# Kernel optimization log

Measured on AMD Instinct MI355X. Metric: run time of the kernel, lower is better.

Reference implementation:

```python
import jax, jax.numpy as jnp
import numpy as np

D_K = 128
NEG = -1e19

def setup_inputs() -> dict:
    key = jax.random.key(0)
    k1, k2, k3 = jax.random.split(key, 3)
    B, H, S, D = 4, 16, 2048, D_K
    return {
        "query": jax.random.normal(k1, (B, H, S, D), dtype=jnp.float32),
        "key": jax.random.normal(k2, (B, H, S, D), dtype=jnp.float32),
        "value": jax.random.normal(k3, (B, H, S, D), dtype=jnp.float32),
    }

def reference(query, key, value):
    # scores: [B,H,S,S]
    scores = jnp.einsum('bhqd,bhkd->bhqk', query, key) / np.sqrt(D_K).astype(np.float32)
    S = scores.shape[-1]
    # causal mask: 1 above diagonal -> add -1e19 (masked_mha=True, training=True path)
    mask = 1.0 - jnp.tril(jnp.ones((S, S), dtype=scores.dtype))
    scores = scores + mask[None, None, :, :] * NEG
    probs = jax.nn.softmax(scores, axis=-1)
    return jnp.einsum('bhqk,bhkd->bhqd', probs, value)
```

## Files before the change

kernel.cpp:

```cpp
#include <hip/hip_runtime.h>
#include <hip/hip_bf16.h>

typedef __attribute__((ext_vector_type(8))) short bf16x8;
typedef __attribute__((ext_vector_type(4))) float f32x4;

#define LOG2E  1.4426950408889634f
#define QSCALE 0.08838834764831845f

__device__ __forceinline__ short f2bf(float f) {
  union { float f; unsigned u; } x;
  x.f = f;
  unsigned u = x.u;
  u += 0x7fffu + ((u >> 16) & 1u);
  return (short)(u >> 16);
}

__device__ __forceinline__ unsigned packbf(float a, float b) {
  return (unsigned)(unsigned short)f2bf(a) | ((unsigned)(unsigned short)f2bf(b) << 16);
}

__global__ __launch_bounds__(256, 2) void attn_fwd(
    const float* __restrict__ Qg, const float* __restrict__ Kg,
    const float* __restrict__ Vg, float* __restrict__ Og)
{
  __shared__ short K_lds[2][64 * 128];
  __shared__ short V_T[2][128 * 64];

  const int tid  = threadIdx.x;
  const int lane = tid & 63;
  const int wave = tid >> 6;
  const int g    = lane >> 4;
  const int lo   = lane & 15;
  const int lo7  = lo & 7;

  const int bh = blockIdx.x;
  const int qt = 15 - blockIdx.y;
  const int q0 = qt * 128;

  const size_t base = (size_t)bh * 2048 * 128;
  const float* Qb = Qg + base;
  const float* Kb = Kg + base;
  const float* Vb = Vg + base;
  float*       Ob = Og + base;

  const int vd   = tid & 31;
  const int vprb = tid >> 5;

  bf16x8 qf[2][4];
  #pragma unroll
  for (int mt = 0; mt < 2; ++mt) {
    const int row = q0 + wave * 32 + mt * 16 + lo;
    const float* qr = Qb + (size_t)row * 128 + g * 8;
    #pragma unroll
    for (int kb = 0; kb < 4; ++kb) {
      f32x4 a = *(const f32x4*)(qr + kb * 32);
      f32x4 b = *(const f32x4*)(qr + kb * 32 + 4);
      bf16x8 w;
      #pragma unroll
      for (int jj = 0; jj < 4; ++jj) { w[jj] = f2bf(a[jj] * QSCALE); w[4 + jj] = f2bf(b[jj] * QSCALE); }
      qf[mt][kb] = w;
    }
  }

  float m_st[2] = {-3.0e38f, -3.0e38f};
  float l_st[2] = {0.0f, 0.0f};
  f32x4 o_acc[2][8];
  #pragma unroll
  for (int mt = 0; mt < 2; ++mt)
    #pragma unroll
    for (int nd = 0; nd < 8; ++nd) o_acc[mt][nd] = (f32x4){0.f, 0.f, 0.f, 0.f};

  const bool b1 = (g >> 1) & 1;
  const bool b0 = g & 1;

  const int ntiles = 2 * (qt + 1);

  {
    #pragma unroll
    for (int i = 0; i < 4; ++i) {
      const int idx = i * 256 + tid;
      const int kr = idx >> 4, dc16 = idx & 15;
      const float* src = Kb + (size_t)kr * 128 + dc16 * 8;
      f32x4 a = *(const f32x4*)src;
      f32x4 b = *(const f32x4*)(src + 4);
      bf16x8 w;
      #pragma unroll
      for (int jj = 0; jj < 4; ++jj) { w[jj] = f2bf(a[jj]); w[4 + jj] = f2bf(b[jj]); }
      *(bf16x8*)&K_lds[0][kr * 128 + ((dc16 ^ (kr & 7)) * 8)] = w;
    }
    #pragma unroll
    for (int i = 0; i < 4; ++i) {
      const int pr = vprb + i * 8;
      const float* v0 = Vb + (size_t)(2 * pr) * 128 + vd;
      #pragma unroll
      for (int jj = 0; jj < 4; ++jj) {
        const int row = vd + jj * 32;
        const unsigned pk = packbf(v0[jj * 32], v0[jj * 32 + 128]);
        *(unsigned*)&V_T[0][row * 64 + (((pr >> 2) ^ (row & 7)) * 8) + (pr & 3) * 2] = pk;
      }
    }
  }
  __syncthreads();

  int cur = 0;
  for (int t = 0; t < ntiles; ++t) {
    const int kv0 = t * 64;
    const short* Kc = K_lds[cur];
    const short* Vc = V_T[cur];
    short* Kn = K_lds[cur ^ 1];
    short* Vn = V_T[cur ^ 1];

    f32x4 kpa[4], kpb[4];
    float vp[4][4][2];
    const bool have_next = (t + 1 < ntiles);
    if (have_next) {
      const int nkv0 = kv0 + 64;
      #pragma unroll
      for (int i = 0; i < 4; ++i) {
        const int idx = i * 256 + tid;
        const int kr = idx >> 4, dc16 = idx & 15;
        const float* src = Kb + (size_t)(nkv0 + kr) * 128 + dc16 * 8;
        kpa[i] = *(const f32x4*)src;
        kpb[i] = *(const f32x4*)(src + 4);
      }
      #pragma unroll
      for (int i = 0; i < 4; ++i) {
        const int pr = vprb + i * 8;
        const float* v0 = Vb + (size_t)(nkv0 + 2 * pr) * 128 + vd;
        #pragma unroll
        for (int jj = 0; jj < 4; ++jj) { vp[i][jj][0] = v0[jj * 32]; vp[i][jj][1] = v0[jj * 32 + 128]; }
      }
    }
    __builtin_amdgcn_sched_barrier(0);

    if (kv0 <= q0 + wave * 32 + 31) {
      f32x4 s[2][4];
      #pragma unroll
      for (int mt = 0; mt < 2; ++mt)
        #pragma unroll
        for (int nb = 0; nb < 4; ++nb) s[mt][nb] = (f32x4){0.f, 0.f, 0.f, 0.f};

      __builtin_amdgcn_s_setprio(1);
      #pragma unroll
      for (int nb = 0; nb < 4; ++nb) {
        #pragma unroll
        for (int kb = 0; kb < 4; ++kb) {
          bf16x8 kf = *(const bf16x8*)&Kc[(nb * 16 + lo) * 128 + (((kb * 4 + g) ^ lo7) * 8)];
          s[0][nb] = __builtin_amdgcn_mfma_f32_16x16x32_bf16(kf, qf[0][kb], s[0][nb], 0, 0, 0);
          s[1][nb] = __builtin_amdgcn_mfma_f32_16x16x32_bf16(kf, qf[1][kb], s[1][nb], 0, 0, 0);
        }
      }
      __builtin_amdgcn_s_setprio(0);

      if (kv0 + 63 > q0 + wave * 32) {
        #pragma unroll
        for (int mt = 0; mt < 2; ++mt) {
          const int qrow = q0 + wave * 32 + mt * 16 + lo;
          #pragma unroll
          for (int nb = 0; nb < 4; ++nb) {
            const int kvb = kv0 + nb * 16 + g * 4;
            #pragma unroll
            for (int r = 0; r < 4; ++r)
              if (kvb + r > qrow) s[mt][nb][r] = -1.0e30f;
          }
        }
      }

      bf16x8 pfrag[2][2];
      #pragma unroll
      for (int mt = 0; mt < 2; ++mt) {
        float tm = s[mt][0][0];
        #pragma unroll
        for (int nb = 0; nb < 4; ++nb)
          #pragma unroll
          for (int r = 0; r < 4; ++r) tm = fmaxf(tm, s[mt][nb][r]);
        tm = fmaxf(tm, __shfl_xor(tm, 16));
        tm = fmaxf(tm, __shfl_xor(tm, 32));
        const float mn = fmaxf(m_st[mt], tm);
        const float alpha = __builtin_amdgcn_exp2f((m_st[mt] - mn) * LOG2E);
        m_st[mt] = mn;

        float p[4][4];
        float ps = 0.0f;
        #pragma unroll
        for (int nb = 0; nb < 4; ++nb)
          #pragma unroll
          for (int r = 0; r < 4; ++r) {
            p[nb][r] = __builtin_amdgcn_exp2f((s[mt][nb][r] - mn) * LOG2E);
            ps += p[nb][r];
          }
        ps += __shfl_xor(ps, 16);
        ps += __shfl_xor(ps, 32);
        l_st[mt] = l_st[mt] * alpha + ps;
        #pragma unroll
        for (int nd = 0; nd < 8; ++nd)
          #pragma unroll
          for (int r = 0; r < 4; ++r) o_acc[mt][nd][r] *= alpha;

        unsigned pk[2][2][2];
        #pragma unroll
        for (int n1 = 0; n1 < 2; ++n1)
          #pragma unroll
          for (int n0 = 0; n0 < 2; ++n0)
            #pragma unroll
            for (int w = 0; w < 2; ++w)
              pk[n1][n0][w] = packbf(p[n1 * 2 + n0][2 * w], p[n1 * 2 + n0][2 * w + 1]);

        #pragma unroll
        for (int n1 = 0; n1 < 2; ++n1) {
          unsigned q2[2][2];
          #pragma unroll
          for (int w = 0; w < 2; ++w) {
            unsigned a = pk[n1][0][w], b = pk[n1][1][w];
            unsigned recv = __shfl_xor(b1 ? a : b, 32);
            unsigned r0 = b1 ? recv : a;
            unsigned r1 = b1 ? b : recv;
            unsigned recv2 = __shfl_xor(b0 ? r0 : r1, 16);
            q2[0][w] = b0 ? recv2 : r0;
            q2[1][w] = b0 ? r1 : recv2;
          }
          union { bf16x8 v; unsigned u[4]; } fb;
          fb.u[0] = q2[0][0]; fb.u[1] = q2[0][1]; fb.u[2] = q2[1][0]; fb.u[3] = q2[1][1];
          pfrag[mt][n1] = fb.v;
        }
      }

      __builtin_amdgcn_s_setprio(1);
      #pragma unroll
      for (int kb2 = 0; kb2 < 2; ++kb2) {
        #pragma unroll
        for (int nd = 0; nd < 8; ++nd) {
          bf16x8 vf = *(const bf16x8*)&Vc[(nd * 16 + lo) * 64 + (((kb2 * 4 + g) ^ lo7) * 8)];
          o_acc[0][nd] = __builtin_amdgcn_mfma_f32_16x16x32_bf16(vf, pfrag[0][kb2], o_acc[0][nd], 0, 0, 0);
          o_acc[1][nd] = __builtin_amdgcn_mfma_f32_16x16x32_bf16(vf, pfrag[1][kb2], o_acc[1][nd], 0, 0, 0);
        }
      }
      __builtin_amdgcn_s_setprio(0);
    }

    if (have_next) {
      #pragma unroll
      for (int i = 0; i < 4; ++i) {
        const int idx = i * 256 + tid;
        const int kr = idx >> 4, dc16 = idx & 15;
        bf16x8 w;
        #pragma unroll
        for (int jj = 0; jj < 4; ++jj) { w[jj] = f2bf(kpa[i][jj]); w[4 + jj] = f2bf(kpb[i][jj]); }
        *(bf16x8*)&Kn[kr * 128 + ((dc16 ^ (kr & 7)) * 8)] = w;
      }
      #pragma unroll
      for (int i = 0; i < 4; ++i) {
        const int pr = vprb + i * 8;
        #pragma unroll
        for (int jj = 0; jj < 4; ++jj) {
          const int row = vd + jj * 32;
          const unsigned pk = packbf(vp[i][jj][0], vp[i][jj][1]);
          *(unsigned*)&Vn[row * 64 + (((pr >> 2) ^ (row & 7)) * 8) + (pr & 3) * 2] = pk;
        }
      }
    }
    __syncthreads();
    cur ^= 1;
  }

  #pragma unroll
  for (int mt = 0; mt < 2; ++mt) {
    const float inv = 1.0f / l_st[mt];
    const int q = q0 + wave * 32 + mt * 16 + lo;
    #pragma unroll
    for (int nd = 0; nd < 8; ++nd) {
      f32x4 o;
      #pragma unroll
      for (int r = 0; r < 4; ++r) o[r] = o_acc[mt][nd][r] * inv;
      *(f32x4*)(Ob + (size_t)q * 128 + nd * 16 + g * 4) = o;
    }
  }
}

extern "C" void kernel_launch(void* const* d_in, const int* in_sizes, int n_in,
                              void* d_out, int out_size, void* d_ws, size_t ws_size,
                              hipStream_t stream) {
  const float* Q = (const float*)d_in[0];
  const float* K = (const float*)d_in[1];
  const float* V = (const float*)d_in[2];
  float* O = (float*)d_out;
  attn_fwd<<<dim3(64, 16), 256, 0, stream>>>(Q, K, V, O);
}
```

Baseline: 155.3 us.

## Use hardware packed bf16 conversion and lazy softmax rescaling with threshold

Replaces the software round-to-nearest bf16 conversion with the v_cvt_pk_bf16_f32 instruction, which packs two floats per instruction. Adds a lazy online-softmax rescale: the running max and the rescaling of the output accumulator and row sum only happen when some row's new max exceeds the stored max by more than a threshold. This is meant to cut VALU work in the softmax and conversion paths. The risk is that exponentials can reach up to 2^(8*log2e) before rescaling, which is still safe in fp32 and bf16.

```diff
diff --git a/kernel.cpp b/kernel.cpp
--- a/kernel.cpp
+++ b/kernel.cpp
@@ -6,17 +6,12 @@
 
 #define LOG2E  1.4426950408889634f
 #define QSCALE 0.08838834764831845f
-
-__device__ __forceinline__ short f2bf(float f) {
-  union { float f; unsigned u; } x;
-  x.f = f;
-  unsigned u = x.u;
-  u += 0x7fffu + ((u >> 16) & 1u);
-  return (short)(u >> 16);
-}
-
-__device__ __forceinline__ unsigned packbf(float a, float b) {
-  return (unsigned)(unsigned short)f2bf(a) | ((unsigned)(unsigned short)f2bf(b) << 16);
+#define DMTHR  8.0f
+
+__device__ __forceinline__ unsigned cvt_pk_bf16(float lo, float hi) {
+  unsigned r;
+  asm("v_cvt_pk_bf16_f32 %0, %1, %2" : "=v"(r) : "v"(lo), "v"(hi));
+  return r;
 }
 
 __global__ __launch_bounds__(256, 2) void attn_fwd(
@@ -55,10 +50,12 @@
     for (int kb = 0; kb < 4; ++kb) {
       f32x4 a = *(const f32x4*)(qr + kb * 32);
       f32x4 b = *(const f32x4*)(qr + kb * 32 + 4);
-      bf16x8 w;
-      #pragma unroll
-      for (int jj = 0; jj < 4; ++jj) { w[jj] = f2bf(a[jj] * QSCALE); w[4 + jj] = f2bf(b[jj] * QSCALE); }
-      qf[mt][kb] = w;
+      union { bf16x8 v; unsigned u[4]; } w;
+      w.u[0] = cvt_pk_bf16(a[0] * QSCALE, a[1] * QSCALE);
+      w.u[1] = cvt_pk_bf16(a[2] * QSCALE, a[3] * QSCALE);
+      w.u[2] = cvt_pk_bf16(b[0] * QSCALE, b[1] * QSCALE);
+      w.u[3] = cvt_pk_bf16(b[2] * QSCALE, b[3] * QSCALE);
+      qf[mt][kb] = w.v;
     }
   }
 
@@ -83,10 +80,12 @@
       const float* src = Kb + (size_t)kr * 128 + dc16 * 8;
       f32x4 a = *(const f32x4*)src;
       f32x4 b = *(const f32x4*)(src + 4);
-      bf16x8 w;
-      #pragma unroll
-      for (int jj = 0; jj < 4; ++jj) { w[jj] = f2bf(a[jj]); w[4 + jj] = f2bf(b[jj]); }
-      *(bf16x8*)&K_lds[0][kr * 128 + ((dc16 ^ (kr & 7)) * 8)] = w;
+      union { bf16x8 v; unsigned u[4]; } w;
+      w.u[0] = cvt_pk_bf16(a[0], a[1]);
+      w.u[1] = cvt_pk_bf16(a[2], a[3]);
+      w.u[2] = cvt_pk_bf16(b[0], b[1]);
+      w.u[3] = cvt_pk_bf16(b[2], b[3]);
+      *(bf16x8*)&K_lds[0][kr * 128 + ((dc16 ^ (kr & 7)) * 8)] = w.v;
     }
     #pragma unroll
     for (int i = 0; i < 4; ++i) {
@@ -95,7 +94,7 @@
       #pragma unroll
       for (int jj = 0; jj < 4; ++jj) {
         const int row = vd + jj * 32;
-        const unsigned pk = packbf(v0[jj * 32], v0[jj * 32 + 128]);
+        const unsigned pk = cvt_pk_bf16(v0[jj * 32], v0[jj * 32 + 128]);
         *(unsigned*)&V_T[0][row * 64 + (((pr >> 2) ^ (row & 7)) * 8) + (pr & 3) * 2] = pk;
       }
     }
@@ -176,9 +175,17 @@
           for (int r = 0; r < 4; ++r) tm = fmaxf(tm, s[mt][nb][r]);
         tm = fmaxf(tm, __shfl_xor(tm, 16));
         tm = fmaxf(tm, __shfl_xor(tm, 32));
-        const float mn = fmaxf(m_st[mt], tm);
-        const float alpha = __builtin_amdgcn_exp2f((m_st[mt] - mn) * LOG2E);
-        m_st[mt] = mn;
+
+        if (!__all(tm <= m_st[mt] + DMTHR)) {
+          const float mn = fmaxf(m_st[mt], tm);
+          const float alpha = __builtin_amdgcn_exp2f((m_st[mt] - mn) * LOG2E);
+          m_st[mt] = mn;
+          l_st[mt] *= alpha;
+          #pragma unroll
+          for (int nd = 0; nd < 8; ++nd)
+            #pragma unroll
+            for (int r = 0; r < 4; ++r) o_acc[mt][nd][r] *= alpha;
+        }
 
         float p[4][4];
         float ps = 0.0f;
@@ -186,16 +193,12 @@
         for (int nb = 0; nb < 4; ++nb)
           #pragma unroll
           for (int r = 0; r < 4; ++r) {
-            p[nb][r] = __builtin_amdgcn_exp2f((s[mt][nb][r] - mn) * LOG2E);
+            p[nb][r] = __builtin_amdgcn_exp2f((s[mt][nb][r] - m_st[mt]) * LOG2E);
             ps += p[nb][r];
           }
         ps += __shfl_xor(ps, 16);
         ps += __shfl_xor(ps, 32);
-        l_st[mt] = l_st[mt] * alpha + ps;
-        #pragma unroll
-        for (int nd = 0; nd < 8; ++nd)
-          #pragma unroll
-          for (int r = 0; r < 4; ++r) o_acc[mt][nd][r] *= alpha;
+        l_st[mt] += ps;
 
         unsigned pk[2][2][2];
         #pragma unroll
@@ -204,7 +207,7 @@
           for (int n0 = 0; n0 < 2; ++n0)
             #pragma unroll
             for (int w = 0; w < 2; ++w)
-              pk[n1][n0][w] = packbf(p[n1 * 2 + n0][2 * w], p[n1 * 2 + n0][2 * w + 1]);
+              pk[n1][n0][w] = cvt_pk_bf16(p[n1 * 2 + n0][2 * w], p[n1 * 2 + n0][2 * w + 1]);
 
         #pragma unroll
         for (int n1 = 0; n1 < 2; ++n1) {
@@ -243,10 +246,12 @@
       for (int i = 0; i < 4; ++i) {
         const int idx = i * 256 + tid;
         const int kr = idx >> 4, dc16 = idx & 15;
-        bf16x8 w;
-        #pragma unroll
-        for (int jj = 0; jj < 4; ++jj) { w[jj] = f2bf(kpa[i][jj]); w[4 + jj] = f2bf(kpb[i][jj]); }
-        *(bf16x8*)&Kn[kr * 128 + ((dc16 ^ (kr & 7)) * 8)] = w;
+        union { bf16x8 v; unsigned u[4]; } w;
+        w.u[0] = cvt_pk_bf16(kpa[i][0], kpa[i][1]);
+        w.u[1] = cvt_pk_bf16(kpa[i][2], kpa[i][3]);
+        w.u[2] = cvt_pk_bf16(kpb[i][0], kpb[i][1]);
+        w.u[3] = cvt_pk_bf16(kpb[i][2], kpb[i][3]);
+        *(bf16x8*)&Kn[kr * 128 + ((dc16 ^ (kr & 7)) * 8)] = w.v;
       }
       #pragma unroll
       for (int i = 0; i < 4; ++i) {
@@ -254,7 +259,7 @@
         #pragma unroll
         for (int jj = 0; jj < 4; ++jj) {
           const int row = vd + jj * 32;
-          const unsigned pk = packbf(vp[i][jj][0], vp[i][jj][1]);
+          const unsigned pk = cvt_pk_bf16(vp[i][jj][0], vp[i][jj][1]);
           *(unsigned*)&Vn[row * 64 + (((pr >> 2) ^ (row & 7)) * 8) + (pr & 3) * 2] = pk;
         }
       }
```

After: 134.5 us. 1.15x faster.
